# Performance work log

Measured on AMD Instinct MI355X. Metric: run time of the kernel, lower is better.

Reference implementation:

```python
import jax, jax.numpy as jnp
import numpy as np

BN_EPS = 1e-5


def _conv_bn_relu(x, w, gamma, beta):
    # 3x3 conv, stride 1, pad 1, no bias, NCHW; BatchNorm in training mode (batch stats)
    y = jax.lax.conv_general_dilated(x, w, (1, 1), ((1, 1), (1, 1)),
                                     dimension_numbers=('NCHW', 'OIHW', 'NCHW'))
    mu = y.mean(axis=(0, 2, 3), keepdims=True)
    var = y.var(axis=(0, 2, 3), keepdims=True)  # biased var, as torch BN uses for normalization
    y = (y - mu) * jax.lax.rsqrt(var + BN_EPS)
    y = y * gamma[None, :, None, None] + beta[None, :, None, None]
    return jax.nn.relu(y)


def setup_inputs() -> dict:
    key = jax.random.key(0)
    ks = jax.random.split(key, 12)
    N, C, h, w, H, W = 64, 256, 8, 8, 32, 32
    OC, NC = 256, 80
    inp = {
        'z_f': jax.random.normal(ks[0], (N, C, h, w), jnp.float32),
        'x_f': jax.random.normal(ks[1], (N, C, H, W), jnp.float32),
        'conv_cls_w': 0.05 * jax.random.normal(ks[2], (OC, C + 1, 3, 3), jnp.float32),
        'bn_cls_g': jnp.ones((OC,), jnp.float32),
        'bn_cls_b': jnp.zeros((OC,), jnp.float32),
        'conv_reg_w': 0.05 * jax.random.normal(ks[3], (OC, C + 1, 3, 3), jnp.float32),
        'bn_reg_g': jnp.ones((OC,), jnp.float32),
        'bn_reg_b': jnp.zeros((OC,), jnp.float32),
        'lin_cls_w': 0.01 * jax.random.normal(ks[4], (NC, OC * h * w), jnp.float32),
        'lin_cls_b': jnp.zeros((NC,), jnp.float32),
        'lin_reg_w': 0.01 * jax.random.normal(ks[5], (4 * NC, OC * H * W), jnp.float32),
        'lin_reg_b': jnp.zeros((4 * NC,), jnp.float32),
    }
    return inp


def reference(z_f, x_f, conv_cls_w, bn_cls_g, bn_cls_b, conv_reg_w, bn_reg_g, bn_reg_b,
              lin_cls_w, lin_cls_b, lin_reg_w, lin_reg_b):
    N, C, h, w = z_f.shape
    H, W = x_f.shape[2], x_f.shape[3]
    z = z_f.reshape(N, C, h * w)            # (N, C, hw)
    x = x_f.reshape(N, C, H * W)            # (N, C, HW)
    zt = z.transpose(0, 2, 1)               # (N, hw, C)
    xt = x.transpose(0, 2, 1)               # (N, HW, C)
    # batched pairwise squared-distance + sigmoid transform
    # NOTE: the original batched (ndim==3) path does NOT divide by sqrt(C)
    xs = jnp.sum(zt * zt, axis=-1)[:, :, None]          # (N, hw, 1)
    ys = jnp.sum(xt * xt, axis=-1)[:, None, :]          # (N, 1, HW)
    d = xs + ys - 2.0 * jnp.einsum('npc,nqc->npq', zt, xt)  # (N, hw, HW)
    d = 4.0 * jax.nn.sigmoid(-d) - 1.0     # == 4/(1+exp(d)) - 1, numerically stable
    dist_t = d.min(axis=1, keepdims=True)                    # (N, 1, HW)
    dist_s = d.min(axis=2, keepdims=True).transpose(0, 2, 1)  # (N, 1, hw)
    feat_cls = jnp.concatenate([dist_s, z], axis=1).reshape(N, C + 1, h, w)
    feat_loc = jnp.concatenate([dist_t, x], axis=1).reshape(N, C + 1, H, W)
    fc = _conv_bn_relu(feat_cls, conv_cls_w, bn_cls_g, bn_cls_b)   # (N, OC, h, w)
    fl = _conv_bn_relu(feat_loc, conv_reg_w, bn_reg_g, bn_reg_b)   # (N, OC, H, W)
    cls = fc.reshape(N, -1) @ lin_cls_w.T + lin_cls_b              # (N, n_classes)
    loc = fl.reshape(N, -1) @ lin_reg_w.T + lin_reg_b              # (N, 4*n_classes)
    return (cls, loc)
```

## Files before the change

kernel.cpp:

```cpp
#include <hip/hip_runtime.h>
#include <math.h>

typedef short short8 __attribute__((ext_vector_type(8)));
typedef float f32x4 __attribute__((ext_vector_type(4)));
typedef unsigned int uint4v __attribute__((ext_vector_type(4)));

#define WS_DS_ENC 0
#define WS_DT     4096
#define WS_SUMS   69632
#define WS_SS     70656
#define WS_YCLS   71680
#define WS_YREG   595968
#define WS_XT     8984576
#define WS_ZT     17373184
#define WS_WTR    17897472
#define WS_WTDR   18192384
#define WS_WTC    18196480
#define WS_WTDC   18491392
#define WS_PART   18495488

__device__ __forceinline__ float dsig(float d) {
    return 4.0f / (1.0f + __expf(d)) - 1.0f;
}
__device__ __forceinline__ unsigned fenc(float f) {
    unsigned u = __float_as_uint(f);
    return (u & 0x80000000u) ? ~u : (u | 0x80000000u);
}
__device__ __forceinline__ float fdec(unsigned e) {
    unsigned u = (e & 0x80000000u) ? (e ^ 0x80000000u) : ~e;
    return __uint_as_float(u);
}
__device__ __forceinline__ unsigned short f2bf(float f) {
    unsigned u = __float_as_uint(f);
    return (unsigned short)((u + 0x7fffu + ((u >> 16) & 1u)) >> 16);
}
__device__ __forceinline__ float bf2f(unsigned short h) {
    return __uint_as_float(((unsigned)h) << 16);
}
__device__ __forceinline__ short8 pack8_trunc(const float* f) {
    uint4v u;
#pragma unroll
    for (int i = 0; i < 4; ++i) {
        unsigned lo = __float_as_uint(f[2 * i]) >> 16;
        unsigned hi = __float_as_uint(f[2 * i + 1]) & 0xffff0000u;
        u[i] = lo | hi;
    }
    return __builtin_bit_cast(short8, u);
}

__global__ void k_init(unsigned* __restrict__ ds_enc, float* __restrict__ sums,
                       float* __restrict__ out_loc, const float* __restrict__ lin_reg_b) {
    int i = blockIdx.x * 256 + threadIdx.x;
    if (i < 4096) ds_enc[i] = 0u;
    if (i < 1024) sums[i] = 0.0f;
    if (i < 20480) out_loc[i] = lin_reg_b[i % 320];
}

__global__ __launch_bounds__(256) void k_xt(const float* __restrict__ x, unsigned short* __restrict__ xt) {
    __shared__ float t[64 * 33];
    const int n = blockIdx.x, row = blockIdx.y;
    const int tid = threadIdx.x;
    for (int c4 = 0; c4 < 4; ++c4) {
        const int ic0 = c4 * 64;
        __syncthreads();
        {
            int icl = tid >> 2, cg = tid & 3;
            const float* src = &x[((n * 256 + ic0 + icl) * 32 + row) * 32 + cg * 8];
            float4 a = *reinterpret_cast<const float4*>(src);
            float4 b = *reinterpret_cast<const float4*>(src + 4);
            float* d = &t[icl * 33 + cg * 8];
            d[0] = a.x; d[1] = a.y; d[2] = a.z; d[3] = a.w;
            d[4] = b.x; d[5] = b.y; d[6] = b.z; d[7] = b.w;
        }
        __syncthreads();
        {
            int col = tid & 31, g = tid >> 5;
            short8 v;
#pragma unroll
            for (int j = 0; j < 8; ++j) v[j] = (short)f2bf(t[(g * 8 + j) * 33 + col]);
            *reinterpret_cast<short8*>(&xt[((n * 32 + row) * 32 + col) * 256 + ic0 + g * 8]) = v;
        }
    }
}

__global__ __launch_bounds__(256) void k_zt(const float* __restrict__ z, unsigned short* __restrict__ zt) {
    __shared__ float t[64 * 65];
    const int n = blockIdx.x;
    const int tid = threadIdx.x;
    for (int c4 = 0; c4 < 4; ++c4) {
        const int ic0 = c4 * 64;
        __syncthreads();
        {
            int icl = tid >> 2, pg = tid & 3;
            const float* src = &z[(n * 256 + ic0 + icl) * 64 + pg * 16];
#pragma unroll
            for (int r = 0; r < 4; ++r) {
                float4 a = *reinterpret_cast<const float4*>(src + r * 4);
                float* d = &t[icl * 65 + pg * 16 + r * 4];
                d[0] = a.x; d[1] = a.y; d[2] = a.z; d[3] = a.w;
            }
        }
        __syncthreads();
        {
            int pos = tid & 63, gg = tid >> 6;
            short8 v0, v1;
#pragma unroll
            for (int j = 0; j < 8; ++j) v0[j] = (short)f2bf(t[(gg * 16 + j) * 65 + pos]);
#pragma unroll
            for (int j = 0; j < 8; ++j) v1[j] = (short)f2bf(t[(gg * 16 + 8 + j) * 65 + pos]);
            unsigned short* d = &zt[(n * 64 + pos) * 256 + ic0 + gg * 16];
            *reinterpret_cast<short8*>(d) = v0;
            *reinterpret_cast<short8*>(d + 8) = v1;
        }
    }
}

__global__ void k_wswz(const float* __restrict__ wr, const float* __restrict__ wc,
                       unsigned short* __restrict__ wtr, unsigned short* __restrict__ wtdr,
                       unsigned short* __restrict__ wtc, unsigned short* __restrict__ wtdc) {
    const int idx = blockIdx.x * 256 + threadIdx.x;
    const float* src = blockIdx.y ? wc : wr;
    unsigned short* dw = blockIdx.y ? wtc : wtr;
    unsigned short* dd = blockIdx.y ? wtdc : wtdr;
    if (idx < 73728) {
        int tap = idx >> 13, rem = idx & 8191;
        int kc = rem >> 10, rem2 = rem & 1023;
        int q = rem2 >> 8, oc = rem2 & 255;
        short8 v;
#pragma unroll
        for (int j = 0; j < 8; ++j) {
            int icg = 1 + kc * 32 + q * 8 + j;
            v[j] = (short)f2bf(src[(oc * 257 + icg) * 9 + tap]);
        }
        *reinterpret_cast<short8*>(&dw[idx * 8]) = v;
    } else if (idx < 74752) {
        int i2 = idx - 73728;
        int q = i2 >> 8, oc = i2 & 255;
        short8 v;
#pragma unroll
        for (int j = 0; j < 8; ++j) {
            int k = q * 8 + j;
            v[j] = (k < 9) ? (short)f2bf(src[(oc * 257) * 9 + k]) : (short)0;
        }
        *reinterpret_cast<short8*>(&dd[i2 * 8]) = v;
    }
}

__global__ __launch_bounds__(256) void k_dist(const float* __restrict__ z, const float* __restrict__ x,
                                              float* __restrict__ dist_t, unsigned* __restrict__ ds_enc) {
    __shared__ float zsq_s[64];
    const int n = blockIdx.y;
    const int q = (blockIdx.x << 8) + threadIdx.x;
    const float* zb = z + n * 16384;
    const float* xb = x + n * 262144;

    if (threadIdx.x < 64) {
        int p = threadIdx.x;
        float s = 0.f;
        for (int c = 0; c < 256; ++c) { float v = zb[c * 64 + p]; s = fmaf(v, v, s); }
        zsq_s[p] = s;
    }
    __syncthreads();

    float4 acc[16];
#pragma unroll
    for (int i = 0; i < 16; ++i) acc[i] = make_float4(0.f, 0.f, 0.f, 0.f);
    float xsq = 0.f;
    for (int c = 0; c < 256; ++c) {
        float xv = xb[c * 1024 + q];
        xsq = fmaf(xv, xv, xsq);
        const float4* z4 = reinterpret_cast<const float4*>(zb + c * 64);
#pragma unroll
        for (int i = 0; i < 16; ++i) {
            float4 zv = z4[i];
            acc[i].x = fmaf(zv.x, xv, acc[i].x);
            acc[i].y = fmaf(zv.y, xv, acc[i].y);
            acc[i].z = fmaf(zv.z, xv, acc[i].z);
            acc[i].w = fmaf(zv.w, xv, acc[i].w);
        }
    }

    const int lane = threadIdx.x & 63;
    float dmax = -1e30f;
    auto do_p = [&](int p, float a) {
        float dr = zsq_s[p] + xsq - 2.f * a;
        dmax = fmaxf(dmax, dr);
        float m = dr;
#pragma unroll
        for (int off = 1; off < 64; off <<= 1) m = fmaxf(m, __shfl_xor(m, off));
        if (lane == 0) atomicMax(&ds_enc[n * 64 + p], fenc(m));
    };
#pragma unroll
    for (int i = 0; i < 16; ++i) {
        do_p(4 * i + 0, acc[i].x);
        do_p(4 * i + 1, acc[i].y);
        do_p(4 * i + 2, acc[i].z);
        do_p(4 * i + 3, acc[i].w);
    }
    dist_t[n * 1024 + q] = dsig(dmax);
}

__global__ __launch_bounds__(256) void k_conv_reg(
    const unsigned short* __restrict__ xt, const float* __restrict__ dist_t,
    const unsigned short* __restrict__ wt, const unsigned short* __restrict__ wtd,
    unsigned short* __restrict__ y, float* __restrict__ sums) {
    __shared__ __align__(16) char smem[17408];
    unsigned short* As = (unsigned short*)smem;
    unsigned short* Ds = (unsigned short*)(smem + 16320);
    float* Ts = (float*)smem;

    const int n = blockIdx.y;
    const int pt = blockIdx.x >> 1, ot = blockIdx.x & 1;
    const int tid = threadIdx.x;
    const int w = tid >> 6, lane = tid & 63;
    const int l15 = lane & 15, q = lane >> 4;
    const int wm = w & 1, wn = w >> 1;
    const int ocW = ot * 128 + wn * 64;

    f32x4 acc[4][4];
#pragma unroll
    for (int mi = 0; mi < 4; ++mi)
#pragma unroll
        for (int ni = 0; ni < 4; ++ni) acc[mi][ni] = (f32x4){0.f, 0.f, 0.f, 0.f};

    for (int f = tid; f < 204; f += 256) {
        int rr = f / 34, cc = f % 34;
        int prow = pt * 4 + rr;
        float v = 0.f;
        if (prow >= 1 && prow <= 32 && cc >= 1 && cc <= 32)
            v = dist_t[n * 1024 + (prow - 1) * 32 + (cc - 1)];
        Ds[f] = f2bf(v);
    }
    __syncthreads();
    {
        short8 ad[4];
#pragma unroll
        for (int mi = 0; mi < 4; ++mi) {
            int m = wm * 64 + mi * 16 + l15;
            int r = m >> 5, c = m & 31;
            short8 v = {0, 0, 0, 0, 0, 0, 0, 0};
#pragma unroll
            for (int j = 0; j < 8; ++j) {
                int k = q * 8 + j;
                if (k < 9) {
                    int ky = k / 3, kx = k % 3;
                    v[j] = (short)Ds[(r + ky) * 34 + (c + kx)];
                }
            }
            ad[mi] = v;
        }
#pragma unroll
        for (int ni = 0; ni < 4; ++ni) {
            short8 b = *reinterpret_cast<const short8*>(&wtd[(q * 256 + ocW + ni * 16 + l15) * 8]);
#pragma unroll
            for (int mi = 0; mi < 4; ++mi)
                acc[mi][ni] = __builtin_amdgcn_mfma_f32_16x16x32_bf16(ad[mi], b, acc[mi][ni], 0, 0, 0);
        }
    }

    for (int kc = 0; kc < 8; ++kc) {
        __syncthreads();
#pragma unroll
        for (int it = 0; it < 4; ++it) {
            int f = tid + 256 * it;
            if (f < 816) {
                int cell = f >> 2, ch = f & 3;
                int rr = cell / 34, cc = cell % 34;
                int prow = pt * 4 + rr;
                short8 v = {0, 0, 0, 0, 0, 0, 0, 0};
                if (prow >= 1 && prow <= 32 && cc >= 1 && cc <= 32)
                    v = *reinterpret_cast<const short8*>(
                        &xt[((n * 32 + prow - 1) * 32 + cc - 1) * 256 + kc * 32 + ch * 8]);
                *reinterpret_cast<short8*>(&As[cell * 40 + ch * 8]) = v;
            }
        }
        __syncthreads();
#pragma unroll
        for (int tap = 0; tap < 9; ++tap) {
            const int ky = tap / 3, kx = tap % 3;
            short8 a[4];
#pragma unroll
            for (int mi = 0; mi < 4; ++mi) {
                int m = wm * 64 + mi * 16 + l15;
                int r = (m >> 5) + ky, c = (m & 31) + kx;
                a[mi] = *reinterpret_cast<const short8*>(&As[(r * 34 + c) * 40 + q * 8]);
            }
            const unsigned short* wb = wt + (size_t)(((tap * 8 + kc) * 4 + q) * 256) * 8;
#pragma unroll
            for (int ni = 0; ni < 4; ++ni) {
                short8 b = *reinterpret_cast<const short8*>(&wb[(ocW + ni * 16 + l15) * 8]);
#pragma unroll
                for (int mi = 0; mi < 4; ++mi)
                    acc[mi][ni] = __builtin_amdgcn_mfma_f32_16x16x32_bf16(a[mi], b, acc[mi][ni], 0, 0, 0);
            }
        }
    }

#pragma unroll
    for (int ni = 0; ni < 4; ++ni) {
        float s = 0.f, qq = 0.f;
#pragma unroll
        for (int mi = 0; mi < 4; ++mi)
#pragma unroll
            for (int e = 0; e < 4; ++e) {
                float v = acc[mi][ni][e];
                s += v; qq = fmaf(v, v, qq);
            }
        s += __shfl_xor(s, 16); s += __shfl_xor(s, 32);
        qq += __shfl_xor(qq, 16); qq += __shfl_xor(qq, 32);
        if (lane < 16) {
            atomicAdd(&sums[512 + ocW + ni * 16 + l15], s);
            atomicAdd(&sums[768 + ocW + ni * 16 + l15], qq);
        }
    }

    __syncthreads();
    float* T = Ts + w * 1088;
#pragma unroll
    for (int mi = 0; mi < 4; ++mi) {
#pragma unroll
        for (int ni = 0; ni < 4; ++ni)
#pragma unroll
            for (int e = 0; e < 4; ++e)
                T[(ni * 16 + l15) * 17 + q * 4 + e] = acc[mi][ni][e];
#pragma unroll
        for (int eo = 0; eo < 16; ++eo) {
            int ocl = eo * 4 + q;
            float v = T[ocl * 17 + l15];
            y[(size_t)n * 262144 + (size_t)(ocW + ocl) * 1024 + pt * 128 + wm * 64 + mi * 16 + l15] = f2bf(v);
        }
    }
}

__global__ __launch_bounds__(256) void k_conv_cls(
    const unsigned short* __restrict__ zt, const unsigned* __restrict__ ds_enc,
    const unsigned short* __restrict__ wt, const unsigned short* __restrict__ wtd,
    unsigned short* __restrict__ y, float* __restrict__ sums) {
    __shared__ __align__(16) char smem[17408];
    unsigned short* As = (unsigned short*)smem;
    unsigned short* Ds = (unsigned short*)(smem + 16000);
    float* Ts = (float*)smem;

    const int n0 = blockIdx.x * 2;
    const int ob = blockIdx.y;
    const int tid = threadIdx.x;
    const int w = tid >> 6, lane = tid & 63;
    const int l15 = lane & 15, q = lane >> 4;
    const int wm = w & 1, wn = w >> 1;
    const int ocW = ob * 128 + wn * 64;

    f32x4 acc[4][4];
#pragma unroll
    for (int mi = 0; mi < 4; ++mi)
#pragma unroll
        for (int ni = 0; ni < 4; ++ni) acc[mi][ni] = (f32x4){0.f, 0.f, 0.f, 0.f};

    for (int f = tid; f < 200; f += 256) {
        int n_l = f / 100, rem = f % 100;
        int rr = rem / 10, cc = rem % 10;
        float v = 0.f;
        if (rr >= 1 && rr <= 8 && cc >= 1 && cc <= 8)
            v = dsig(fdec(ds_enc[(n0 + n_l) * 64 + (rr - 1) * 8 + (cc - 1)]));
        Ds[f] = f2bf(v);
    }
    __syncthreads();
    {
        short8 ad[4];
#pragma unroll
        for (int mi = 0; mi < 4; ++mi) {
            int pos = mi * 16 + l15;
            int r = pos >> 3, c = pos & 7;
            short8 v = {0, 0, 0, 0, 0, 0, 0, 0};
#pragma unroll
            for (int j = 0; j < 8; ++j) {
                int k = q * 8 + j;
                if (k < 9) {
                    int ky = k / 3, kx = k % 3;
                    v[j] = (short)Ds[wm * 100 + (r + ky) * 10 + (c + kx)];
                }
            }
            ad[mi] = v;
        }
#pragma unroll
        for (int ni = 0; ni < 4; ++ni) {
            short8 b = *reinterpret_cast<const short8*>(&wtd[(q * 256 + ocW + ni * 16 + l15) * 8]);
#pragma unroll
            for (int mi = 0; mi < 4; ++mi)
                acc[mi][ni] = __builtin_amdgcn_mfma_f32_16x16x32_bf16(ad[mi], b, acc[mi][ni], 0, 0, 0);
        }
    }

    for (int kc = 0; kc < 8; ++kc) {
        __syncthreads();
#pragma unroll
        for (int it = 0; it < 4; ++it) {
            int f = tid + 256 * it;
            if (f < 800) {
                int cell = f >> 2, ch = f & 3;
                int n_l = cell / 100, rem = cell % 100;
                int rr = rem / 10, cc = rem % 10;
                short8 v = {0, 0, 0, 0, 0, 0, 0, 0};
                if (rr >= 1 && rr <= 8 && cc >= 1 && cc <= 8)
                    v = *reinterpret_cast<const short8*>(
                        &zt[((n0 + n_l) * 64 + (rr - 1) * 8 + (cc - 1)) * 256 + kc * 32 + ch * 8]);
                *reinterpret_cast<short8*>(&As[cell * 40 + ch * 8]) = v;
            }
        }
        __syncthreads();
#pragma unroll
        for (int tap = 0; tap < 9; ++tap) {
            const int ky = tap / 3, kx = tap % 3;
            short8 a[4];
#pragma unroll
            for (int mi = 0; mi < 4; ++mi) {
                int pos = mi * 16 + l15;
                int r = (pos >> 3) + ky, c = (pos & 7) + kx;
                a[mi] = *reinterpret_cast<const short8*>(&As[(wm * 100 + r * 10 + c) * 40 + q * 8]);
            }
            const unsigned short* wb = wt + (size_t)(((tap * 8 + kc) * 4 + q) * 256) * 8;
#pragma unroll
            for (int ni = 0; ni < 4; ++ni) {
                short8 b = *reinterpret_cast<const short8*>(&wb[(ocW + ni * 16 + l15) * 8]);
#pragma unroll
                for (int mi = 0; mi < 4; ++mi)
                    acc[mi][ni] = __builtin_amdgcn_mfma_f32_16x16x32_bf16(a[mi], b, acc[mi][ni], 0, 0, 0);
            }
        }
    }

#pragma unroll
    for (int ni = 0; ni < 4; ++ni) {
        float s = 0.f, qq = 0.f;
#pragma unroll
        for (int mi = 0; mi < 4; ++mi)
#pragma unroll
            for (int e = 0; e < 4; ++e) {
                float v = acc[mi][ni][e];
                s += v; qq = fmaf(v, v, qq);
            }
        s += __shfl_xor(s, 16); s += __shfl_xor(s, 32);
        qq += __shfl_xor(qq, 16); qq += __shfl_xor(qq, 32);
        if (lane < 16) {
            atomicAdd(&sums[0 + ocW + ni * 16 + l15], s);
            atomicAdd(&sums[256 + ocW + ni * 16 + l15], qq);
        }
    }

    __syncthreads();
    float* T = Ts + w * 1088;
#pragma unroll
    for (int mi = 0; mi < 4; ++mi) {
#pragma unroll
        for (int ni = 0; ni < 4; ++ni)
#pragma unroll
            for (int e = 0; e < 4; ++e)
                T[(ni * 16 + l15) * 17 + q * 4 + e] = acc[mi][ni][e];
#pragma unroll
        for (int eo = 0; eo < 16; ++eo) {
            int ocl = eo * 4 + q;
            float v = T[ocl * 17 + l15];
            y[(size_t)(n0 + wm) * 16384 + (size_t)(ocW + ocl) * 64 + mi * 16 + l15] = f2bf(v);
        }
    }
}

__global__ void k_bnfin(const float* __restrict__ sums,
                        const float* __restrict__ g_cls, const float* __restrict__ b_cls,
                        const float* __restrict__ g_reg, const float* __restrict__ b_reg,
                        float* __restrict__ ss) {
    int t = threadIdx.x;
    {
        float mean = sums[t] * (1.f / 4096.f);
        float var = sums[256 + t] * (1.f / 4096.f) - mean * mean;
        float sc = g_cls[t] * rsqrtf(var + 1e-5f);
        ss[t] = sc;
        ss[256 + t] = b_cls[t] - mean * sc;
    }
    {
        float mean = sums[512 + t] * (1.f / 65536.f);
        float var = sums[768 + t] * (1.f / 65536.f) - mean * mean;
        float sc = g_reg[t] * rsqrtf(var + 1e-5f);
        ss[512 + t] = sc;
        ss[768 + t] = b_reg[t] - mean * sc;
    }
}

__global__ __launch_bounds__(256) void k_lin_cls(const unsigned short* __restrict__ y, const float* __restrict__ ss,
                                                 const float* __restrict__ w, const float* __restrict__ bias,
                                                 float* __restrict__ out) {
    const int jt = blockIdx.x, n = blockIdx.y, j0 = jt * 16;
    const int tid = threadIdx.x;
    float part[16];
#pragma unroll
    for (int j = 0; j < 16; ++j) part[j] = 0.f;

    for (int s = 0; s < 8; ++s) {
        int k8 = (s * 256 + tid) * 8;
        short8 yv = *reinterpret_cast<const short8*>(&y[n * 16384 + k8]);
        int ch = k8 >> 6;
        float sc = ss[ch], sh = ss[256 + ch];
        float a_[8];
#pragma unroll
        for (int j = 0; j < 8; ++j)
            a_[j] = fmaxf(fmaf(bf2f((unsigned short)yv[j]), sc, sh), 0.f);
#pragma unroll
        for (int j = 0; j < 16; ++j) {
            const float* wp = &w[(j0 + j) * 16384 + k8];
            float4 w0 = *reinterpret_cast<const float4*>(wp);
            float4 w1 = *reinterpret_cast<const float4*>(wp + 4);
            float p = part[j];
            p = fmaf(a_[0], w0.x, p); p = fmaf(a_[1], w0.y, p);
            p = fmaf(a_[2], w0.z, p); p = fmaf(a_[3], w0.w, p);
            p = fmaf(a_[4], w1.x, p); p = fmaf(a_[5], w1.y, p);
            p = fmaf(a_[6], w1.z, p); p = fmaf(a_[7], w1.w, p);
            part[j] = p;
        }
    }
    __shared__ float red[16][4];
    const int lane = tid & 63, wid = tid >> 6;
#pragma unroll
    for (int j = 0; j < 16; ++j) {
        float v = part[j];
#pragma unroll
        for (int off = 1; off < 64; off <<= 1) v += __shfl_xor(v, off);
        if (lane == 0) red[j][wid] = v;
    }
    __syncthreads();
    if (tid < 16)
        out[n * 80 + j0 + tid] = red[tid][0] + red[tid][1] + red[tid][2] + red[tid][3] + bias[j0 + tid];
}

__global__ __launch_bounds__(256) void k_lin_reg2(const unsigned short* __restrict__ y, const float* __restrict__ ss,
                                                  const float* __restrict__ w, float* __restrict__ part) {
    __shared__ __align__(16) unsigned short A_l[32 * 520];
    const int k0 = blockIdx.x * 512;
    const int tid = threadIdx.x;
    const int wv = tid >> 6, lane = tid & 63;
    const int l15 = lane & 15, q = lane >> 4;
    const int jw = wv * 80;

    f32x4 acc[5][4];
#pragma unroll
    for (int ni = 0; ni < 5; ++ni)
#pragma unroll
        for (int mi = 0; mi < 4; ++mi) acc[ni][mi] = (f32x4){0.f, 0.f, 0.f, 0.f};

    for (int scn = 0; scn < 2; ++scn) {
        const int ksub = k0 + scn * 256;
        const int ch = ksub >> 10;
        const float scf = ss[512 + ch], shf = ss[768 + ch];
        __syncthreads();
        {
            const int c = tid & 31, nb = tid >> 5;
#pragma unroll
            for (int p = 0; p < 8; ++p) {
                const int n = p * 8 + nb;
                short8 v = *reinterpret_cast<const short8*>(&y[(size_t)n * 262144 + ksub + c * 8]);
                float f[8];
#pragma unroll
                for (int j = 0; j < 8; ++j)
                    f[j] = fmaxf(fmaf(bf2f((unsigned short)v[j]), scf, shf), 0.f);
                *reinterpret_cast<short8*>(&A_l[c * 520 + n * 8]) = pack8_trunc(f);
            }
        }
        __syncthreads();
#pragma unroll
        for (int kk = 0; kk < 8; ++kk) {
            short8 a[4];
#pragma unroll
            for (int mi = 0; mi < 4; ++mi)
                a[mi] = *reinterpret_cast<const short8*>(&A_l[(kk * 4 + q) * 520 + (mi * 16 + l15) * 8]);
            short8 b[5];
#pragma unroll
            for (int ni = 0; ni < 5; ++ni) {
                const float* wp = &w[(size_t)(jw + ni * 16 + l15) * 262144 + ksub + kk * 32 + q * 8];
                float4 b0 = *reinterpret_cast<const float4*>(wp);
                float4 b1 = *reinterpret_cast<const float4*>(wp + 4);
                float f[8] = {b0.x, b0.y, b0.z, b0.w, b1.x, b1.y, b1.z, b1.w};
                b[ni] = pack8_trunc(f);
            }
#pragma unroll
            for (int ni = 0; ni < 5; ++ni)
#pragma unroll
                for (int mi = 0; mi < 4; ++mi)
                    acc[ni][mi] = __builtin_amdgcn_mfma_f32_16x16x32_bf16(a[mi], b[ni], acc[ni][mi], 0, 0, 0);
        }
    }

    float* pb = part + (size_t)blockIdx.x * 20480;
#pragma unroll
    for (int ni = 0; ni < 5; ++ni) {
        const int j = jw + ni * 16 + l15;
#pragma unroll
        for (int mi = 0; mi < 4; ++mi)
#pragma unroll
            for (int e = 0; e < 4; ++e) {
                const int n = mi * 16 + q * 4 + e;
                pb[n * 320 + j] = acc[ni][mi][e];
            }
    }
}

__global__ __launch_bounds__(256) void k_lin_red(const float* __restrict__ part, float* __restrict__ out_loc) {
    const int idx = blockIdx.x * 256 + threadIdx.x;
    const int b0 = blockIdx.y * 128;
    float s0 = 0.f, s1 = 0.f, s2 = 0.f, s3 = 0.f;
#pragma unroll 4
    for (int b = 0; b < 128; b += 4) {
        s0 += part[(size_t)(b0 + b + 0) * 20480 + idx];
        s1 += part[(size_t)(b0 + b + 1) * 20480 + idx];
        s2 += part[(size_t)(b0 + b + 2) * 20480 + idx];
        s3 += part[(size_t)(b0 + b + 3) * 20480 + idx];
    }
    atomicAdd(&out_loc[idx], (s0 + s1) + (s2 + s3));
}

extern "C" void kernel_launch(void* const* d_in, const int* in_sizes, int n_in,
                              void* d_out, int out_size, void* d_ws, size_t ws_size,
                              hipStream_t stream) {
    const float* z_f        = (const float*)d_in[0];
    const float* x_f        = (const float*)d_in[1];
    const float* conv_cls_w = (const float*)d_in[2];
    const float* bn_cls_g   = (const float*)d_in[3];
    const float* bn_cls_b   = (const float*)d_in[4];
    const float* conv_reg_w = (const float*)d_in[5];
    const float* bn_reg_g   = (const float*)d_in[6];
    const float* bn_reg_b   = (const float*)d_in[7];
    const float* lin_cls_w  = (const float*)d_in[8];
    const float* lin_cls_b  = (const float*)d_in[9];
    const float* lin_reg_w  = (const float*)d_in[10];
    const float* lin_reg_b  = (const float*)d_in[11];

    float* out = (float*)d_out;
    float* ws  = (float*)d_ws;
    unsigned* ds_enc = (unsigned*)(ws + WS_DS_ENC);
    float* dist_t = ws + WS_DT;
    float* sums   = ws + WS_SUMS;
    float* ss     = ws + WS_SS;
    unsigned short* y_cls = (unsigned short*)(ws + WS_YCLS);
    unsigned short* y_reg = (unsigned short*)(ws + WS_YREG);
    unsigned short* xt    = (unsigned short*)(ws + WS_XT);
    unsigned short* zt    = (unsigned short*)(ws + WS_ZT);
    unsigned short* wtr   = (unsigned short*)(ws + WS_WTR);
    unsigned short* wtdr  = (unsigned short*)(ws + WS_WTDR);
    unsigned short* wtc   = (unsigned short*)(ws + WS_WTC);
    unsigned short* wtdc  = (unsigned short*)(ws + WS_WTDC);
    float* part   = ws + WS_PART;

    hipLaunchKernelGGL(k_init, dim3(80), dim3(256), 0, stream, ds_enc, sums, out + 5120, lin_reg_b);
    hipLaunchKernelGGL(k_xt, dim3(64, 32), dim3(256), 0, stream, x_f, xt);
    hipLaunchKernelGGL(k_zt, dim3(64), dim3(256), 0, stream, z_f, zt);
    hipLaunchKernelGGL(k_wswz, dim3(292, 2), dim3(256), 0, stream, conv_reg_w, conv_cls_w, wtr, wtdr, wtc, wtdc);
    hipLaunchKernelGGL(k_dist, dim3(4, 64), dim3(256), 0, stream, z_f, x_f, dist_t, ds_enc);
    hipLaunchKernelGGL(k_conv_reg, dim3(16, 64), dim3(256), 0, stream, xt, dist_t, wtr, wtdr, y_reg, sums);
    hipLaunchKernelGGL(k_conv_cls, dim3(32, 2), dim3(256), 0, stream, zt, ds_enc, wtc, wtdc, y_cls, sums);
    hipLaunchKernelGGL(k_bnfin, dim3(1), dim3(256), 0, stream, sums, bn_cls_g, bn_cls_b, bn_reg_g, bn_reg_b, ss);
    hipLaunchKernelGGL(k_lin_cls, dim3(5, 64), dim3(256), 0, stream, y_cls, ss, lin_cls_w, lin_cls_b, out);
    hipLaunchKernelGGL(k_lin_reg2, dim3(512), dim3(256), 0, stream, y_reg, ss, lin_reg_w, part);
    hipLaunchKernelGGL(k_lin_red, dim3(80, 4), dim3(256), 0, stream, part, out + 5120);
}
```

Before: 917.1 us.

## Use bf16 MFMA for distance matrix and cls linear, fuse squared norms

Rewrites the pairwise-distance kernel to use bf16 MFMA tiles over the pre-transposed bf16 activations instead of scalar fp32 FMAs. Row squared norms are now computed as a side product of the transpose kernels. The classification linear layer becomes a split-K MFMA kernel that accumulates into a bias-initialised output with atomics. This removes a large scalar-FMA workload, but lowers dot-product precision to bf16, which can shift the min-distance selection near ties.

```diff
diff --git a/kernel.cpp b/kernel.cpp
--- a/kernel.cpp
+++ b/kernel.cpp
@@ -18,6 +18,8 @@
 #define WS_WTC    18196480
 #define WS_WTDC   18491392
 #define WS_PART   18495488
+#define WS_XSQ    28981248
+#define WS_ZSQ    29046784
 
 __device__ __forceinline__ float dsig(float d) {
     return 4.0f / (1.0f + __expf(d)) - 1.0f;
@@ -49,17 +51,23 @@
 }
 
 __global__ void k_init(unsigned* __restrict__ ds_enc, float* __restrict__ sums,
-                       float* __restrict__ out_loc, const float* __restrict__ lin_reg_b) {
+                       float* __restrict__ out_cls, float* __restrict__ out_loc,
+                       const float* __restrict__ lin_cls_b, const float* __restrict__ lin_reg_b) {
     int i = blockIdx.x * 256 + threadIdx.x;
     if (i < 4096) ds_enc[i] = 0u;
     if (i < 1024) sums[i] = 0.0f;
+    if (i < 5120) out_cls[i] = lin_cls_b[i % 80];
     if (i < 20480) out_loc[i] = lin_reg_b[i % 320];
 }
 
-__global__ __launch_bounds__(256) void k_xt(const float* __restrict__ x, unsigned short* __restrict__ xt) {
+__global__ __launch_bounds__(256) void k_xt(const float* __restrict__ x, unsigned short* __restrict__ xt,
+                                            float* __restrict__ xsq) {
     __shared__ float t[64 * 33];
+    __shared__ float xr[4][32];
     const int n = blockIdx.x, row = blockIdx.y;
     const int tid = threadIdx.x;
+    const int col = tid & 31, g = tid >> 5;
+    float sq = 0.f;
     for (int c4 = 0; c4 < 4; ++c4) {
         const int ic0 = c4 * 64;
         __syncthreads();
@@ -74,19 +82,30 @@
         }
         __syncthreads();
         {
-            int col = tid & 31, g = tid >> 5;
             short8 v;
 #pragma unroll
-            for (int j = 0; j < 8; ++j) v[j] = (short)f2bf(t[(g * 8 + j) * 33 + col]);
+            for (int j = 0; j < 8; ++j) {
+                float f = t[(g * 8 + j) * 33 + col];
+                sq = fmaf(f, f, sq);
+                v[j] = (short)f2bf(f);
+            }
             *reinterpret_cast<short8*>(&xt[((n * 32 + row) * 32 + col) * 256 + ic0 + g * 8]) = v;
         }
     }
-}
-
-__global__ __launch_bounds__(256) void k_zt(const float* __restrict__ z, unsigned short* __restrict__ zt) {
+    sq += __shfl_xor(sq, 32);
+    if ((tid & 63) < 32) xr[tid >> 6][col] = sq;
+    __syncthreads();
+    if (tid < 32) xsq[(n * 32 + row) * 32 + tid] = xr[0][tid] + xr[1][tid] + xr[2][tid] + xr[3][tid];
+}
+
+__global__ __launch_bounds__(256) void k_zt(const float* __restrict__ z, unsigned short* __restrict__ zt,
+                                            float* __restrict__ zsq) {
     __shared__ float t[64 * 65];
+    __shared__ float zr[4][64];
     const int n = blockIdx.x;
     const int tid = threadIdx.x;
+    const int pos = tid & 63, gg = tid >> 6;
+    float sq = 0.f;
     for (int c4 = 0; c4 < 4; ++c4) {
         const int ic0 = c4 * 64;
         __syncthreads();
@@ -102,17 +121,27 @@
         }
         __syncthreads();
         {
-            int pos = tid & 63, gg = tid >> 6;
             short8 v0, v1;
 #pragma unroll
-            for (int j = 0; j < 8; ++j) v0[j] = (short)f2bf(t[(gg * 16 + j) * 65 + pos]);
-#pragma unroll
-            for (int j = 0; j < 8; ++j) v1[j] = (short)f2bf(t[(gg * 16 + 8 + j) * 65 + pos]);
+            for (int j = 0; j < 8; ++j) {
+                float f = t[(gg * 16 + j) * 65 + pos];
+                sq = fmaf(f, f, sq);
+                v0[j] = (short)f2bf(f);
+            }
+#pragma unroll
+            for (int j = 0; j < 8; ++j) {
+                float f = t[(gg * 16 + 8 + j) * 65 + pos];
+                sq = fmaf(f, f, sq);
+                v1[j] = (short)f2bf(f);
+            }
             unsigned short* d = &zt[(n * 64 + pos) * 256 + ic0 + gg * 16];
             *reinterpret_cast<short8*>(d) = v0;
             *reinterpret_cast<short8*>(d + 8) = v1;
         }
     }
+    zr[gg][pos] = sq;
+    __syncthreads();
+    if (tid < 64) zsq[n * 64 + tid] = zr[0][tid] + zr[1][tid] + zr[2][tid] + zr[3][tid];
 }
 
 __global__ void k_wswz(const float* __restrict__ wr, const float* __restrict__ wc,
@@ -146,58 +175,74 @@
     }
 }
 
-__global__ __launch_bounds__(256) void k_dist(const float* __restrict__ z, const float* __restrict__ x,
+__global__ __launch_bounds__(256) void k_dist(const unsigned short* __restrict__ zt,
+                                              const unsigned short* __restrict__ xt,
+                                              const float* __restrict__ zsq, const float* __restrict__ xsq,
                                               float* __restrict__ dist_t, unsigned* __restrict__ ds_enc) {
-    __shared__ float zsq_s[64];
     const int n = blockIdx.y;
-    const int q = (blockIdx.x << 8) + threadIdx.x;
-    const float* zb = z + n * 16384;
-    const float* xb = x + n * 262144;
-
-    if (threadIdx.x < 64) {
-        int p = threadIdx.x;
-        float s = 0.f;
-        for (int c = 0; c < 256; ++c) { float v = zb[c * 64 + p]; s = fmaf(v, v, s); }
-        zsq_s[p] = s;
-    }
-    __syncthreads();
-
-    float4 acc[16];
-#pragma unroll
-    for (int i = 0; i < 16; ++i) acc[i] = make_float4(0.f, 0.f, 0.f, 0.f);
-    float xsq = 0.f;
-    for (int c = 0; c < 256; ++c) {
-        float xv = xb[c * 1024 + q];
-        xsq = fmaf(xv, xv, xsq);
-        const float4* z4 = reinterpret_cast<const float4*>(zb + c * 64);
-#pragma unroll
-        for (int i = 0; i < 16; ++i) {
-            float4 zv = z4[i];
-            acc[i].x = fmaf(zv.x, xv, acc[i].x);
-            acc[i].y = fmaf(zv.y, xv, acc[i].y);
-            acc[i].z = fmaf(zv.z, xv, acc[i].z);
-            acc[i].w = fmaf(zv.w, xv, acc[i].w);
-        }
-    }
-
-    const int lane = threadIdx.x & 63;
-    float dmax = -1e30f;
-    auto do_p = [&](int p, float a) {
-        float dr = zsq_s[p] + xsq - 2.f * a;
-        dmax = fmaxf(dmax, dr);
-        float m = dr;
-#pragma unroll
-        for (int off = 1; off < 64; off <<= 1) m = fmaxf(m, __shfl_xor(m, off));
-        if (lane == 0) atomicMax(&ds_enc[n * 64 + p], fenc(m));
-    };
-#pragma unroll
-    for (int i = 0; i < 16; ++i) {
-        do_p(4 * i + 0, acc[i].x);
-        do_p(4 * i + 1, acc[i].y);
-        do_p(4 * i + 2, acc[i].z);
-        do_p(4 * i + 3, acc[i].w);
-    }
-    dist_t[n * 1024 + q] = dsig(dmax);
+    const int tid = threadIdx.x;
+    const int wv = tid >> 6, lane = tid & 63;
+    const int l15 = lane & 15, q4 = lane >> 4;
+    const int q0 = blockIdx.x * 256 + wv * 64;
+    const unsigned short* zb = zt + n * 16384;
+    const unsigned short* xb = xt + (size_t)(n * 1024 + q0) * 256;
+
+    f32x4 acc[4][4];
+#pragma unroll
+    for (int mi = 0; mi < 4; ++mi)
+#pragma unroll
+        for (int ni = 0; ni < 4; ++ni) acc[mi][ni] = (f32x4){0.f, 0.f, 0.f, 0.f};
+
+#pragma unroll
+    for (int ks = 0; ks < 8; ++ks) {
+        short8 a[4], b[4];
+#pragma unroll
+        for (int mi = 0; mi < 4; ++mi)
+            a[mi] = *reinterpret_cast<const short8*>(&zb[(mi * 16 + l15) * 256 + ks * 32 + q4 * 8]);
+#pragma unroll
+        for (int ni = 0; ni < 4; ++ni)
+            b[ni] = *reinterpret_cast<const short8*>(&xb[(ni * 16 + l15) * 256 + ks * 32 + q4 * 8]);
+#pragma unroll
+        for (int ni = 0; ni < 4; ++ni)
+#pragma unroll
+            for (int mi = 0; mi < 4; ++mi)
+                acc[mi][ni] = __builtin_amdgcn_mfma_f32_16x16x32_bf16(a[mi], b[ni], acc[mi][ni], 0, 0, 0);
+    }
+
+    float zs[4][4];
+#pragma unroll
+    for (int mi = 0; mi < 4; ++mi)
+#pragma unroll
+        for (int e = 0; e < 4; ++e) zs[mi][e] = zsq[n * 64 + mi * 16 + q4 * 4 + e];
+    float xq[4];
+#pragma unroll
+    for (int ni = 0; ni < 4; ++ni) xq[ni] = xsq[n * 1024 + q0 + ni * 16 + l15];
+
+#pragma unroll
+    for (int ni = 0; ni < 4; ++ni) {
+        float m = -1e30f;
+#pragma unroll
+        for (int mi = 0; mi < 4; ++mi)
+#pragma unroll
+            for (int e = 0; e < 4; ++e)
+                m = fmaxf(m, zs[mi][e] - 2.f * acc[mi][ni][e]);
+        m = fmaxf(m, __shfl_xor(m, 16));
+        m = fmaxf(m, __shfl_xor(m, 32));
+        if (lane < 16) dist_t[n * 1024 + q0 + ni * 16 + l15] = dsig(m + xq[ni]);
+    }
+#pragma unroll
+    for (int mi = 0; mi < 4; ++mi)
+#pragma unroll
+        for (int e = 0; e < 4; ++e) {
+            float v = -1e30f;
+#pragma unroll
+            for (int ni = 0; ni < 4; ++ni) v = fmaxf(v, xq[ni] - 2.f * acc[mi][ni][e]);
+            v = fmaxf(v, __shfl_xor(v, 1));
+            v = fmaxf(v, __shfl_xor(v, 2));
+            v = fmaxf(v, __shfl_xor(v, 4));
+            v = fmaxf(v, __shfl_xor(v, 8));
+            if (l15 == 0) atomicMax(&ds_enc[n * 64 + mi * 16 + q4 * 4 + e], fenc(zs[mi][e] + v));
+        }
 }
 
 __global__ __launch_bounds__(256) void k_conv_reg(
@@ -486,48 +531,38 @@
 }
 
 __global__ __launch_bounds__(256) void k_lin_cls(const unsigned short* __restrict__ y, const float* __restrict__ ss,
-                                                 const float* __restrict__ w, const float* __restrict__ bias,
-                                                 float* __restrict__ out) {
-    const int jt = blockIdx.x, n = blockIdx.y, j0 = jt * 16;
+                                                 const float* __restrict__ w, float* __restrict__ out) {
+    const int kb = blockIdx.x * 256;
     const int tid = threadIdx.x;
-    float part[16];
-#pragma unroll
-    for (int j = 0; j < 16; ++j) part[j] = 0.f;
-
-    for (int s = 0; s < 8; ++s) {
-        int k8 = (s * 256 + tid) * 8;
-        short8 yv = *reinterpret_cast<const short8*>(&y[n * 16384 + k8]);
-        int ch = k8 >> 6;
-        float sc = ss[ch], sh = ss[256 + ch];
-        float a_[8];
-#pragma unroll
-        for (int j = 0; j < 8; ++j)
-            a_[j] = fmaxf(fmaf(bf2f((unsigned short)yv[j]), sc, sh), 0.f);
-#pragma unroll
-        for (int j = 0; j < 16; ++j) {
-            const float* wp = &w[(j0 + j) * 16384 + k8];
-            float4 w0 = *reinterpret_cast<const float4*>(wp);
-            float4 w1 = *reinterpret_cast<const float4*>(wp + 4);
-            float p = part[j];
-            p = fmaf(a_[0], w0.x, p); p = fmaf(a_[1], w0.y, p);
-            p = fmaf(a_[2], w0.z, p); p = fmaf(a_[3], w0.w, p);
-            p = fmaf(a_[4], w1.x, p); p = fmaf(a_[5], w1.y, p);
-            p = fmaf(a_[6], w1.z, p); p = fmaf(a_[7], w1.w, p);
-            part[j] = p;
-        }
-    }
-    __shared__ float red[16][4];
-    const int lane = tid & 63, wid = tid >> 6;
-#pragma unroll
-    for (int j = 0; j < 16; ++j) {
-        float v = part[j];
-#pragma unroll
-        for (int off = 1; off < 64; off <<= 1) v += __shfl_xor(v, off);
-        if (lane == 0) red[j][wid] = v;
-    }
-    __syncthreads();
-    if (tid < 16)
-        out[n * 80 + j0 + tid] = red[tid][0] + red[tid][1] + red[tid][2] + red[tid][3] + bias[j0 + tid];
+    const int wv = tid >> 6, lane = tid & 63;
+    const int l15 = lane & 15, q4 = lane >> 4;
+    f32x4 acc[5];
+#pragma unroll
+    for (int ni = 0; ni < 5; ++ni) acc[ni] = (f32x4){0.f, 0.f, 0.f, 0.f};
+#pragma unroll
+    for (int ks = 0; ks < 8; ++ks) {
+        const int k0 = kb + ks * 32 + q4 * 8;
+        short8 yv = *reinterpret_cast<const short8*>(&y[(wv * 16 + l15) * 16384 + k0]);
+        const int ch = k0 >> 6;
+        const float sc = ss[ch], sh = ss[256 + ch];
+        float f[8];
+#pragma unroll
+        for (int j = 0; j < 8; ++j) f[j] = fmaxf(fmaf(bf2f((unsigned short)yv[j]), sc, sh), 0.f);
+        short8 a = pack8_trunc(f);
+#pragma unroll
+        for (int ni = 0; ni < 5; ++ni) {
+            const float* wp = &w[(size_t)(ni * 16 + l15) * 16384 + k0];
+            float4 b0 = *reinterpret_cast<const float4*>(wp);
+            float4 b1 = *reinterpret_cast<const float4*>(wp + 4);
+            float g[8] = {b0.x, b0.y, b0.z, b0.w, b1.x, b1.y, b1.z, b1.w};
+            acc[ni] = __builtin_amdgcn_mfma_f32_16x16x32_bf16(a, pack8_trunc(g), acc[ni], 0, 0, 0);
+        }
+    }
+#pragma unroll
+    for (int ni = 0; ni < 5; ++ni)
+#pragma unroll
+        for (int e = 0; e < 4; ++e)
+            atomicAdd(&out[(wv * 16 + q4 * 4 + e) * 80 + ni * 16 + l15], acc[ni][e]);
 }
 
 __global__ __launch_bounds__(256) void k_lin_reg2(const unsigned short* __restrict__ y, const float* __restrict__ ss,
@@ -646,16 +681,18 @@
     unsigned short* wtc   = (unsigned short*)(ws + WS_WTC);
     unsigned short* wtdc  = (unsigned short*)(ws + WS_WTDC);
     float* part   = ws + WS_PART;
-
-    hipLaunchKernelGGL(k_init, dim3(80), dim3(256), 0, stream, ds_enc, sums, out + 5120, lin_reg_b);
-    hipLaunchKernelGGL(k_xt, dim3(64, 32), dim3(256), 0, stream, x_f, xt);
-    hipLaunchKernelGGL(k_zt, dim3(64), dim3(256), 0, stream, z_f, zt);
+    float* xsq    = ws + WS_XSQ;
+    float* zsq    = ws + WS_ZSQ;
+
+    hipLaunchKernelGGL(k_init, dim3(80), dim3(256), 0, stream, ds_enc, sums, out, out + 5120, lin_cls_b, lin_reg_b);
+    hipLaunchKernelGGL(k_xt, dim3(64, 32), dim3(256), 0, stream, x_f, xt, xsq);
+    hipLaunchKernelGGL(k_zt, dim3(64), dim3(256), 0, stream, z_f, zt, zsq);
     hipLaunchKernelGGL(k_wswz, dim3(292, 2), dim3(256), 0, stream, conv_reg_w, conv_cls_w, wtr, wtdr, wtc, wtdc);
-    hipLaunchKernelGGL(k_dist, dim3(4, 64), dim3(256), 0, stream, z_f, x_f, dist_t, ds_enc);
+    hipLaunchKernelGGL(k_dist, dim3(4, 64), dim3(256), 0, stream, zt, xt, zsq, xsq, dist_t, ds_enc);
     hipLaunchKernelGGL(k_conv_reg, dim3(16, 64), dim3(256), 0, stream, xt, dist_t, wtr, wtdr, y_reg, sums);
     hipLaunchKernelGGL(k_conv_cls, dim3(32, 2), dim3(256), 0, stream, zt, ds_enc, wtc, wtdc, y_cls, sums);
     hipLaunchKernelGGL(k_bnfin, dim3(1), dim3(256), 0, stream, sums, bn_cls_g, bn_cls_b, bn_reg_g, bn_reg_b, ss);
-    hipLaunchKernelGGL(k_lin_cls, dim3(5, 64), dim3(256), 0, stream, y_cls, ss, lin_cls_w, lin_cls_b, out);
+    hipLaunchKernelGGL(k_lin_cls, dim3(64), dim3(256), 0, stream, y_cls, ss, lin_cls_w, out);
     hipLaunchKernelGGL(k_lin_reg2, dim3(512), dim3(256), 0, stream, y_reg, ss, lin_reg_w, part);
     hipLaunchKernelGGL(k_lin_red, dim3(80, 4), dim3(256), 0, stream, part, out + 5120);
 }
```

Result: faster. 791.7 us (-13.7%).
